# Performance work log

Measured on AMD Instinct MI355X. Metric: run time of the kernel, lower is better.

## Reference

```python
import jax, jax.numpy as jnp
import numpy as np

B, T, I, H = 64, 2048, 64, 256


def setup_inputs() -> dict:
    key = jax.random.key(0)
    ks = jax.random.split(key, 7)
    s_ih = 1.0 / np.sqrt(H)
    return {
        "x": jax.random.normal(ks[0], (B, T, I), dtype=jnp.float32),
        "W_ih": jax.random.normal(ks[1], (H, I), dtype=jnp.float32) * s_ih,
        "W_hh": jax.random.normal(ks[2], (H, H), dtype=jnp.float32) * s_ih,
        "b_ih": jax.random.normal(ks[3], (H,), dtype=jnp.float32) * s_ih,
        "b_hh": jax.random.normal(ks[4], (H,), dtype=jnp.float32) * s_ih,
        "W_fc": jax.random.normal(ks[5], (1, H), dtype=jnp.float32) * s_ih,
        "b_fc": jax.random.normal(ks[6], (1,), dtype=jnp.float32) * s_ih,
    }


def reference(x, W_ih, W_hh, b_ih, b_hh, W_fc, b_fc):
    # Precompute input projection for all timesteps: [B,T,H]
    pre = jnp.einsum('bti,hi->bth', x, W_ih) + b_ih + b_hh
    pre_t = jnp.swapaxes(pre, 0, 1)  # [T,B,H]

    def step(h, p_t):
        h_new = jnp.tanh(p_t + h @ W_hh.T)
        return h_new, h_new

    h0 = jnp.zeros((x.shape[0], W_hh.shape[0]), dtype=x.dtype)
    _, hs = jax.lax.scan(step, h0, pre_t)  # hs: [T,B,H]
    out = jnp.swapaxes(hs, 0, 1)  # [B,T,H]
    return out @ W_fc.T + b_fc  # [B,T,1]
```

## Files before the change

### kernel.cpp

```cpp
#include <hip/hip_runtime.h>

#define BB 64
#define TT 2048
#define II 64
#define HH 256
#define NTHR 256

typedef _Float16 v8h __attribute__((ext_vector_type(8)));
typedef float v4f __attribute__((ext_vector_type(4)));
typedef int v4i __attribute__((ext_vector_type(4)));

#define PK(a, b) __builtin_bit_cast(int, __builtin_amdgcn_cvt_pkrtz((a), (b)))
#define MFMA __builtin_amdgcn_mfma_f32_16x16x32_f16

__device__ __forceinline__ float ftanh(float x) {
    float e = __expf(2.0f * x);
    return 1.0f - 2.0f * __builtin_amdgcn_rcpf(e + 1.0f);
}

template <int CTRL>
__device__ __forceinline__ float dpp_add(float v) {
    int s = __builtin_amdgcn_update_dpp(0, __float_as_int(v), CTRL, 0xF, 0xF, true);
    return v + __int_as_float(s);
}

__device__ __forceinline__ v8h xfrag(const float4 s0, const float4 s1) {
    v4i r = {PK(s0.x, s0.y), PK(s0.z, s0.w), PK(s1.x, s1.y), PK(s1.z, s1.w)};
    return __builtin_bit_cast(v8h, r);
}

__launch_bounds__(NTHR, 1)
__global__ void rnn_fused(const float* __restrict__ x,
                          const float* __restrict__ W_ih,
                          const float* __restrict__ W_hh,
                          const float* __restrict__ b_ih,
                          const float* __restrict__ b_hh,
                          const float* __restrict__ W_fc,
                          const float* __restrict__ b_fc,
                          float* __restrict__ out) {
    __shared__ __align__(16) __fp16 hlds[2][HH];
    __shared__ float part[TT + 1][4];

    const int tid  = threadIdx.x;
    const int b    = blockIdx.x;
    const int lane = tid & 63;
    const int w    = tid >> 6;
    const int g    = lane >> 4;
    const int c16  = lane & 15;

    v8h bf[4][10];
    v4f bvv[4];
    float wf[4];
#pragma unroll
    for (int tc = 0; tc < 4; ++tc) {
        const int n = 64 * w + 16 * tc + c16;
#pragma unroll
        for (int T = 0; T < 8; ++T) {
            const float* wp = W_hh + n * HH + 32 * T + 8 * g;
            const float4 f0 = *(const float4*)wp;
            const float4 f1 = *(const float4*)(wp + 4);
            v4i r = {PK(f0.x, f0.y), PK(f0.z, f0.w), PK(f1.x, f1.y), PK(f1.z, f1.w)};
            bf[tc][T] = __builtin_bit_cast(v8h, r);
        }
#pragma unroll
        for (int T = 8; T < 10; ++T) {
            const float* wp = W_ih + n * II + 32 * (T - 8) + 8 * g;
            const float4 f0 = *(const float4*)wp;
            const float4 f1 = *(const float4*)(wp + 4);
            v4i r = {PK(f0.x, f0.y), PK(f0.z, f0.w), PK(f1.x, f1.y), PK(f1.z, f1.w)};
            bf[tc][T] = __builtin_bit_cast(v8h, r);
        }
        const float bias = b_ih[n] + b_hh[n];
        bvv[tc] = (v4f){bias, bias, bias, bias};
        wf[tc] = W_fc[n];
    }
    v4f zq = (v4f){0.f, 0.f, 0.f, 0.f};
#pragma unroll
    for (int tc = 0; tc < 4; ++tc) {
#pragma unroll
        for (int T = 0; T < 10; ++T) asm volatile("" : "+v"(bf[tc][T]));
        asm volatile("" : "+v"(bvv[tc]));
        asm volatile("" : "+v"(wf[tc]));
    }
    asm volatile("" : "+v"(zq));
    const float bfc = b_fc[0];

    for (int idx = tid; idx < 2 * HH; idx += NTHR)
        ((__fp16*)hlds)[idx] = (__fp16)0;
    __syncthreads();

    const float* xrow = x + (size_t)b * TT * II;
    float* outb = out + (size_t)b * TT;

    const char* hrd0 = (const char*)&hlds[0][0] + g * 16;
    const char* hrd1 = (const char*)&hlds[1][0] + g * 16;
    __fp16* hwr0 = &hlds[0][64 * w + c16];
    __fp16* hwr1 = &hlds[1][64 * w + c16];

    v8h xf8, xf9;
    float4 rA0, rA1, rA2, rA3, rB0, rB1, rB2, rB3;
    {
        const float* x0 = xrow;
        xf8 = xfrag(*(const float4*)(x0 + 8 * g), *(const float4*)(x0 + 8 * g + 4));
        xf9 = xfrag(*(const float4*)(x0 + 32 + 8 * g), *(const float4*)(x0 + 36 + 8 * g));
        const float* x1 = xrow + II;
        rA0 = *(const float4*)(x1 + 8 * g);      rA1 = *(const float4*)(x1 + 8 * g + 4);
        rA2 = *(const float4*)(x1 + 32 + 8 * g); rA3 = *(const float4*)(x1 + 36 + 8 * g);
        const float* x2 = xrow + 2 * II;
        rB0 = *(const float4*)(x2 + 8 * g);      rB1 = *(const float4*)(x2 + 8 * g + 4);
        rB2 = *(const float4*)(x2 + 32 + 8 * g); rB3 = *(const float4*)(x2 + 36 + 8 * g);
    }

    float ph = 0.0f;

#define STEP(I, P, R0, R1, R2, R3)                                             \
    {                                                                          \
                  \
        const char* hrd = (P) ? hrd1 : hrd0;                                   \
        const v8h hv0 = *(const v8h*)(hrd + 0 * 64);                           \
        const v8h hv1 = *(const v8h*)(hrd + 1 * 64);                           \
        const v8h hv2 = *(const v8h*)(hrd + 2 * 64);                           \
        const v8h hv3 = *(const v8h*)(hrd + 3 * 64);                           \
        const v8h hv4 = *(const v8h*)(hrd + 4 * 64);                           \
        const v8h hv5 = *(const v8h*)(hrd + 5 * 64);                           \
        const v8h hv6 = *(const v8h*)(hrd + 6 * 64);                           \
        const v8h hv7 = *(const v8h*)(hrd + 7 * 64);                           \
        \
        if ((I) > 0) {                                                         \
            float hc = ph;                                                     \
            hc = dpp_add<0xB1>(hc);                                            \
            hc = dpp_add<0x4E>(hc);                                            \
            hc = dpp_add<0x141>(hc);                                           \
            hc = dpp_add<0x140>(hc);                                           \
            if (lane == 0) part[I][w] = hc;                                    \
        }                                                                      \
                   \
        v4f aA0 = MFMA(xf8, bf[0][8], bvv[0], 0, 0, 0);                        \
        v4f aA1 = MFMA(xf8, bf[1][8], bvv[1], 0, 0, 0);                        \
        v4f aA2 = MFMA(xf8, bf[2][8], bvv[2], 0, 0, 0);                        \
        v4f aA3 = MFMA(xf8, bf[3][8], bvv[3], 0, 0, 0);                        \
        aA0 = MFMA(xf9, bf[0][9], aA0, 0, 0, 0);                               \
        aA1 = MFMA(xf9, bf[1][9], aA1, 0, 0, 0);                               \
        aA2 = MFMA(xf9, bf[2][9], aA2, 0, 0, 0);                               \
        aA3 = MFMA(xf9, bf[3][9], aA3, 0, 0, 0);                               \
        aA0 = MFMA(hv0, bf[0][0], aA0, 0, 0, 0);                               \
        aA1 = MFMA(hv0, bf[1][0], aA1, 0, 0, 0);                               \
        aA2 = MFMA(hv0, bf[2][0], aA2, 0, 0, 0);                               \
        aA3 = MFMA(hv0, bf[3][0], aA3, 0, 0, 0);                               \
        aA0 = MFMA(hv1, bf[0][1], aA0, 0, 0, 0);                               \
        aA1 = MFMA(hv1, bf[1][1], aA1, 0, 0, 0);                               \
        aA2 = MFMA(hv1, bf[2][1], aA2, 0, 0, 0);                               \
        aA3 = MFMA(hv1, bf[3][1], aA3, 0, 0, 0);                               \
                  \
        v4f aB0 = MFMA(hv2, bf[0][2], zq, 0, 0, 0);                            \
        v4f aB1 = MFMA(hv2, bf[1][2], zq, 0, 0, 0);                            \
        v4f aB2 = MFMA(hv2, bf[2][2], zq, 0, 0, 0);                            \
        v4f aB3 = MFMA(hv2, bf[3][2], zq, 0, 0, 0);                            \
        aB0 = MFMA(hv3, bf[0][3], aB0, 0, 0, 0);                               \
        aB1 = MFMA(hv3, bf[1][3], aB1, 0, 0, 0);                               \
        aB2 = MFMA(hv3, bf[2][3], aB2, 0, 0, 0);                               \
        aB3 = MFMA(hv3, bf[3][3], aB3, 0, 0, 0);                               \
        aB0 = MFMA(hv4, bf[0][4], aB0, 0, 0, 0);                               \
        aB1 = MFMA(hv4, bf[1][4], aB1, 0, 0, 0);                               \
        aB2 = MFMA(hv4, bf[2][4], aB2, 0, 0, 0);                               \
        aB3 = MFMA(hv4, bf[3][4], aB3, 0, 0, 0);                               \
                  \
        v4f aC0 = MFMA(hv5, bf[0][5], zq, 0, 0, 0);                            \
        v4f aC1 = MFMA(hv5, bf[1][5], zq, 0, 0, 0);                            \
        v4f aC2 = MFMA(hv5, bf[2][5], zq, 0, 0, 0);                            \
        v4f aC3 = MFMA(hv5, bf[3][5], zq, 0, 0, 0);                            \
        aC0 = MFMA(hv6, bf[0][6], aC0, 0, 0, 0);                               \
        aC1 = MFMA(hv6, bf[1][6], aC1, 0, 0, 0);                               \
        aC2 = MFMA(hv6, bf[2][6], aC2, 0, 0, 0);                               \
        aC3 = MFMA(hv6, bf[3][6], aC3, 0, 0, 0);                               \
        aC0 = MFMA(hv7, bf[0][7], aC0, 0, 0, 0);                               \
        aC1 = MFMA(hv7, bf[1][7], aC1, 0, 0, 0);                               \
        aC2 = MFMA(hv7, bf[2][7], aC2, 0, 0, 0);                               \
        aC3 = MFMA(hv7, bf[3][7], aC3, 0, 0, 0);                               \
           \
        xf8 = xfrag(R0, R1);                                                   \
        xf9 = xfrag(R2, R3);                                                   \
        {                                                                      \
            const int rn = ((I) + 3 < TT) ? ((I) + 3) : (TT - 1);              \
            const float* xp = xrow + rn * II;                                  \
            R0 = *(const float4*)(xp + 8 * g);                                 \
            R1 = *(const float4*)(xp + 8 * g + 4);                             \
            R2 = *(const float4*)(xp + 32 + 8 * g);                            \
            R3 = *(const float4*)(xp + 36 + 8 * g);                            \
        }                                                                      \
         \
        const float h0 = ftanh(aA0[0] + aB0[0] + aC0[0]);                      \
        const float h1 = ftanh(aA1[0] + aB1[0] + aC1[0]);                      \
        const float h2 = ftanh(aA2[0] + aB2[0] + aC2[0]);                      \
        const float h3 = ftanh(aA3[0] + aB3[0] + aC3[0]);                      \
        ph = fmaf(h3, wf[3], fmaf(h2, wf[2], fmaf(h1, wf[1], h0 * wf[0])));    \
        if (lane < 16) {                                                       \
            __fp16* hp = (P) ? hwr0 : hwr1;                                    \
            hp[0]  = (__fp16)h0;                                               \
            hp[16] = (__fp16)h1;                                               \
            hp[32] = (__fp16)h2;                                               \
            hp[48] = (__fp16)h3;                                               \
        }                                                                      \
             \
        asm volatile("s_waitcnt lgkmcnt(0)\n\ts_barrier" ::: "memory");        \
    }

    for (int ib = 0; ib < TT; ib += 2) {
        STEP(ib, 0, rA0, rA1, rA2, rA3)
        STEP(ib + 1, 1, rB0, rB1, rB2, rB3)
    }
#undef STEP

    {
        float hc = ph;
        hc = dpp_add<0xB1>(hc);
        hc = dpp_add<0x4E>(hc);
        hc = dpp_add<0x141>(hc);
        hc = dpp_add<0x140>(hc);
        if (lane == 0) part[TT][w] = hc;
    }
    __syncthreads();

    for (int i = tid; i < TT; i += NTHR) {
        const float4 s = *(const float4*)&part[i + 1][0];
        outb[i] = s.x + s.y + s.z + s.w + bfc;
    }
}

extern "C" void kernel_launch(void* const* d_in, const int* in_sizes, int n_in,
                              void* d_out, int out_size, void* d_ws, size_t ws_size,
                              hipStream_t stream) {
    const float* x    = (const float*)d_in[0];
    const float* W_ih = (const float*)d_in[1];
    const float* W_hh = (const float*)d_in[2];
    const float* b_ih = (const float*)d_in[3];
    const float* b_hh = (const float*)d_in[4];
    const float* W_fc = (const float*)d_in[5];
    const float* b_fc = (const float*)d_in[6];
    float* out = (float*)d_out;

    rnn_fused<<<BB, NTHR, 0, stream>>>(x, W_ih, W_hh, b_ih, b_hh, W_fc, b_fc, out);
}
```

Measured before the change: 1.318 ms.

## Split recurrent hidden columns across eight waves instead of four

Doubles the block to 512 threads so each wave computes 32 hidden units (two 16-column MFMA tiles) per timestep instead of 64. The MFMA sequence is reorganized into two interleaved accumulator chains per tile. The partial-sum buffer for the output projection is widened to eight entries per step to match. The aim is to shorten each wave's per-step critical path and let waves sharing a SIMD hide each other's latency. In exchange, the per-step barrier spans twice as many waves and the LDS footprint grows, while the MFMA work per SIMD stays the same.

```diff
diff --git a/kernel.cpp b/kernel.cpp
--- a/kernel.cpp
+++ b/kernel.cpp
@@ -4,7 +4,7 @@
 #define TT 2048
 #define II 64
 #define HH 256
-#define NTHR 256
+#define NTHR 512
 
 typedef _Float16 v8h __attribute__((ext_vector_type(8)));
 typedef float v4f __attribute__((ext_vector_type(4)));
@@ -29,7 +29,7 @@
     return __builtin_bit_cast(v8h, r);
 }
 
-__launch_bounds__(NTHR, 1)
+__launch_bounds__(NTHR, 2)
 __global__ void rnn_fused(const float* __restrict__ x,
                           const float* __restrict__ W_ih,
                           const float* __restrict__ W_hh,
@@ -39,7 +39,7 @@
                           const float* __restrict__ b_fc,
                           float* __restrict__ out) {
     __shared__ __align__(16) __fp16 hlds[2][HH];
-    __shared__ float part[TT + 1][4];
+    __shared__ float part[TT + 1][8];
 
     const int tid  = threadIdx.x;
     const int b    = blockIdx.x;
@@ -48,12 +48,12 @@
     const int g    = lane >> 4;
     const int c16  = lane & 15;
 
-    v8h bf[4][10];
-    v4f bvv[4];
-    float wf[4];
-#pragma unroll
-    for (int tc = 0; tc < 4; ++tc) {
-        const int n = 64 * w + 16 * tc + c16;
+    v8h bf[2][10];
+    v4f bvv[2];
+    float wf[2];
+#pragma unroll
+    for (int tc = 0; tc < 2; ++tc) {
+        const int n = 32 * w + 16 * tc + c16;
 #pragma unroll
         for (int T = 0; T < 8; ++T) {
             const float* wp = W_hh + n * HH + 32 * T + 8 * g;
@@ -76,7 +76,7 @@
     }
     v4f zq = (v4f){0.f, 0.f, 0.f, 0.f};
 #pragma unroll
-    for (int tc = 0; tc < 4; ++tc) {
+    for (int tc = 0; tc < 2; ++tc) {
 #pragma unroll
         for (int T = 0; T < 10; ++T) asm volatile("" : "+v"(bf[tc][T]));
         asm volatile("" : "+v"(bvv[tc]));
@@ -94,8 +94,8 @@
 
     const char* hrd0 = (const char*)&hlds[0][0] + g * 16;
     const char* hrd1 = (const char*)&hlds[1][0] + g * 16;
-    __fp16* hwr0 = &hlds[0][64 * w + c16];
-    __fp16* hwr1 = &hlds[1][64 * w + c16];
+    __fp16* hwr0 = &hlds[0][32 * w + c16];
+    __fp16* hwr1 = &hlds[1][32 * w + c16];
 
     v8h xf8, xf9;
     float4 rA0, rA1, rA2, rA3, rB0, rB1, rB2, rB3;
@@ -134,49 +134,27 @@
             hc = dpp_add<0x140>(hc);                                           \
             if (lane == 0) part[I][w] = hc;                                    \
         }                                                                      \
-                   \
+               \
         v4f aA0 = MFMA(xf8, bf[0][8], bvv[0], 0, 0, 0);                        \
         v4f aA1 = MFMA(xf8, bf[1][8], bvv[1], 0, 0, 0);                        \
-        v4f aA2 = MFMA(xf8, bf[2][8], bvv[2], 0, 0, 0);                        \
-        v4f aA3 = MFMA(xf8, bf[3][8], bvv[3], 0, 0, 0);                        \
+        v4f aB0 = MFMA(hv3, bf[0][3], zq, 0, 0, 0);                            \
+        v4f aB1 = MFMA(hv3, bf[1][3], zq, 0, 0, 0);                            \
         aA0 = MFMA(xf9, bf[0][9], aA0, 0, 0, 0);                               \
         aA1 = MFMA(xf9, bf[1][9], aA1, 0, 0, 0);                               \
-        aA2 = MFMA(xf9, bf[2][9], aA2, 0, 0, 0);                               \
-        aA3 = MFMA(xf9, bf[3][9], aA3, 0, 0, 0);                               \
+        aB0 = MFMA(hv4, bf[0][4], aB0, 0, 0, 0);                               \
+        aB1 = MFMA(hv4, bf[1][4], aB1, 0, 0, 0);                               \
         aA0 = MFMA(hv0, bf[0][0], aA0, 0, 0, 0);                               \
         aA1 = MFMA(hv0, bf[1][0], aA1, 0, 0, 0);                               \
-        aA2 = MFMA(hv0, bf[2][0], aA2, 0, 0, 0);                               \
-        aA3 = MFMA(hv0, bf[3][0], aA3, 0, 0, 0);                               \
+        aB0 = MFMA(hv5, bf[0][5], aB0, 0, 0, 0);                               \
+        aB1 = MFMA(hv5, bf[1][5], aB1, 0, 0, 0);                               \
         aA0 = MFMA(hv1, bf[0][1], aA0, 0, 0, 0);                               \
         aA1 = MFMA(hv1, bf[1][1], aA1, 0, 0, 0);                               \
-        aA2 = MFMA(hv1, bf[2][1], aA2, 0, 0, 0);                               \
-        aA3 = MFMA(hv1, bf[3][1], aA3, 0, 0, 0);                               \
-                  \
-        v4f aB0 = MFMA(hv2, bf[0][2], zq, 0, 0, 0);                            \
-        v4f aB1 = MFMA(hv2, bf[1][2], zq, 0, 0, 0);                            \
-        v4f aB2 = MFMA(hv2, bf[2][2], zq, 0, 0, 0);                            \
-        v4f aB3 = MFMA(hv2, bf[3][2], zq, 0, 0, 0);                            \
-        aB0 = MFMA(hv3, bf[0][3], aB0, 0, 0, 0);                               \
-        aB1 = MFMA(hv3, bf[1][3], aB1, 0, 0, 0);                               \
-        aB2 = MFMA(hv3, bf[2][3], aB2, 0, 0, 0);                               \
-        aB3 = MFMA(hv3, bf[3][3], aB3, 0, 0, 0);                               \
-        aB0 = MFMA(hv4, bf[0][4], aB0, 0, 0, 0);                               \
-        aB1 = MFMA(hv4, bf[1][4], aB1, 0, 0, 0);                               \
-        aB2 = MFMA(hv4, bf[2][4], aB2, 0, 0, 0);                               \
-        aB3 = MFMA(hv4, bf[3][4], aB3, 0, 0, 0);                               \
-                  \
-        v4f aC0 = MFMA(hv5, bf[0][5], zq, 0, 0, 0);                            \
-        v4f aC1 = MFMA(hv5, bf[1][5], zq, 0, 0, 0);                            \
-        v4f aC2 = MFMA(hv5, bf[2][5], zq, 0, 0, 0);                            \
-        v4f aC3 = MFMA(hv5, bf[3][5], zq, 0, 0, 0);                            \
-        aC0 = MFMA(hv6, bf[0][6], aC0, 0, 0, 0);                               \
-        aC1 = MFMA(hv6, bf[1][6], aC1, 0, 0, 0);                               \
-        aC2 = MFMA(hv6, bf[2][6], aC2, 0, 0, 0);                               \
-        aC3 = MFMA(hv6, bf[3][6], aC3, 0, 0, 0);                               \
-        aC0 = MFMA(hv7, bf[0][7], aC0, 0, 0, 0);                               \
-        aC1 = MFMA(hv7, bf[1][7], aC1, 0, 0, 0);                               \
-        aC2 = MFMA(hv7, bf[2][7], aC2, 0, 0, 0);                               \
-        aC3 = MFMA(hv7, bf[3][7], aC3, 0, 0, 0);                               \
+        aB0 = MFMA(hv6, bf[0][6], aB0, 0, 0, 0);                               \
+        aB1 = MFMA(hv6, bf[1][6], aB1, 0, 0, 0);                               \
+        aA0 = MFMA(hv2, bf[0][2], aA0, 0, 0, 0);                               \
+        aA1 = MFMA(hv2, bf[1][2], aA1, 0, 0, 0);                               \
+        aB0 = MFMA(hv7, bf[0][7], aB0, 0, 0, 0);                               \
+        aB1 = MFMA(hv7, bf[1][7], aB1, 0, 0, 0);                               \
            \
         xf8 = xfrag(R0, R1);                                                   \
         xf9 = xfrag(R2, R3);                                                   \
@@ -189,17 +167,13 @@
             R3 = *(const float4*)(xp + 36 + 8 * g);                            \
         }                                                                      \
          \
-        const float h0 = ftanh(aA0[0] + aB0[0] + aC0[0]);                      \
-        const float h1 = ftanh(aA1[0] + aB1[0] + aC1[0]);                      \
-        const float h2 = ftanh(aA2[0] + aB2[0] + aC2[0]);                      \
-        const float h3 = ftanh(aA3[0] + aB3[0] + aC3[0]);                      \
-        ph = fmaf(h3, wf[3], fmaf(h2, wf[2], fmaf(h1, wf[1], h0 * wf[0])));    \
+        const float h0 = ftanh(aA0[0] + aB0[0]);                               \
+        const float h1 = ftanh(aA1[0] + aB1[0]);                               \
+        ph = fmaf(h1, wf[1], h0 * wf[0]);                                      \
         if (lane < 16) {                                                       \
             __fp16* hp = (P) ? hwr0 : hwr1;                                    \
             hp[0]  = (__fp16)h0;                                               \
             hp[16] = (__fp16)h1;                                               \
-            hp[32] = (__fp16)h2;                                               \
-            hp[48] = (__fp16)h3;                                               \
         }                                                                      \
              \
         asm volatile("s_waitcnt lgkmcnt(0)\n\ts_barrier" ::: "memory");        \
@@ -222,8 +196,9 @@
     __syncthreads();
 
     for (int i = tid; i < TT; i += NTHR) {
-        const float4 s = *(const float4*)&part[i + 1][0];
-        outb[i] = s.x + s.y + s.z + s.w + bfc;
+        const float4 s0 = *(const float4*)&part[i + 1][0];
+        const float4 s1 = *(const float4*)&part[i + 1][4];
+        outb[i] = s0.x + s0.y + s0.z + s0.w + s1.x + s1.y + s1.z + s1.w + bfc;
     }
 }
 
```

New measurement: 1.171 ms. -11.2%, faster.
